# Kernel tuning notes

Hardware: AMD Instinct MI355X
Metric: run time of the kernel (lower is better)

Reference implementation:

```python
import jax, jax.numpy as jnp
from jax import lax
import numpy as np

T = 8
TAU = 2.0       # LIFNode tau
VTH = 1.0       # v_threshold for IF and LIF
ALPHA = 2.0     # surrogate.ATan default alpha
BN_EPS = 1e-5

# --- ATan surrogate-gradient heaviside (spikingjelly semantics) ---
@jax.custom_vjp
def heaviside_atan(x):
    return (x >= 0.0).astype(x.dtype)

def _h_fwd(x):
    return heaviside_atan(x), x

def _h_bwd(x, g):
    sg = (ALPHA / 2.0) / (1.0 + (jnp.pi / 2.0 * ALPHA * x) ** 2)
    return (g * sg,)

heaviside_atan.defvjp(_h_fwd, _h_bwd)

# --- multi-step IF node: v += x; spike; hard reset to 0 ---
def if_node(x_seq):
    def step(v, x):
        v = v + x
        s = heaviside_atan(v - VTH)
        return (1.0 - s) * v, s
    return lax.scan(step, jnp.zeros_like(x_seq[0]), x_seq)[1]

# --- multi-step LIF node (decay_input=True, v_reset=0, hard reset) ---
def lif_node(x_seq):
    def step(v, x):
        v = v + (x - v) / TAU
        s = heaviside_atan(v - VTH)
        return (1.0 - s) * v, s
    return lax.scan(step, jnp.zeros_like(x_seq[0]), x_seq)[1]

def conv2d(x, w, b):
    y = lax.conv_general_dilated(x, w, (1, 1), 'SAME', dimension_numbers=('NCHW', 'OIHW', 'NCHW'))
    return y + b[None, :, None, None]

def bn(x, g, b, m, v):
    scale = g * lax.rsqrt(v + BN_EPS)
    return (x - m[None, :, None, None]) * scale[None, :, None, None] + b[None, :, None, None]

def maxpool2(x):
    return lax.reduce_window(x, -jnp.inf, lax.max, (1, 1, 2, 2), (1, 1, 2, 2), 'VALID')


def setup_inputs():
    key = jax.random.key(0)
    ks = jax.random.split(key, 8)
    B = 32
    f32 = jnp.float32
    d = {}
    d['x'] = jax.random.normal(ks[0], (B, 1, 48, 48), f32)
    d['conv1_w'] = jax.random.normal(ks[1], (128, 1, 3, 3), f32) * 0.2
    d['conv1_b'] = jnp.zeros((128,), f32)
    d['bn1_g'] = jnp.ones((128,), f32)
    d['bn1_b'] = jnp.zeros((128,), f32)
    d['bn1_m'] = jnp.zeros((128,), f32)
    d['bn1_v'] = jnp.ones((128,), f32)
    d['conv2_w'] = jax.random.normal(ks[2], (128, 128, 3, 3), f32) * 0.03
    d['conv2_b'] = jnp.zeros((128,), f32)
    d['bn2_g'] = jnp.ones((128,), f32)
    d['bn2_b'] = jnp.zeros((128,), f32)
    d['bn2_m'] = jnp.zeros((128,), f32)
    d['bn2_v'] = jnp.ones((128,), f32)
    d['fc1_w'] = jax.random.normal(ks[3], (1152, 128 * 12 * 12), f32) * 0.007
    d['fc1_b'] = jnp.zeros((1152,), f32)
    d['fc2_w'] = jax.random.normal(ks[4], (128, 1152), f32) * 0.03
    d['fc2_b'] = jnp.zeros((128,), f32)
    d['fc3_w'] = jax.random.normal(ks[5], (7, 128), f32) * 0.09
    d['fc3_b'] = jnp.zeros((7,), f32)
    return d


def reference(x, conv1_w, conv1_b, bn1_g, bn1_b, bn1_m, bn1_v,
              conv2_w, conv2_b, bn2_g, bn2_b, bn2_m, bn2_v,
              fc1_w, fc1_b, fc2_w, fc2_b, fc3_w, fc3_b):
    B = x.shape[0]
    # layer1 (single-step): conv + BN (eval-mode), dropout is identity at eval
    h = bn(conv2d(x, conv1_w, conv1_b), bn1_g, bn1_b, bn1_m, bn1_v)  # [B,128,48,48]
    # repeat over T timesteps
    x_step = jnp.broadcast_to(h, (T,) + h.shape)                      # [T,B,128,48,48]
    # layer2: IF -> maxpool -> conv -> BN -> IF -> maxpool
    s1 = if_node(x_step)                                              # [T,B,128,48,48]
    p1 = maxpool2(s1.reshape((T * B,) + s1.shape[2:]))                # [T*B,128,24,24]
    c2 = bn(conv2d(p1, conv2_w, conv2_b), bn2_g, bn2_b, bn2_m, bn2_v)
    s2 = if_node(c2.reshape((T, B) + c2.shape[1:]))                   # [T,B,128,24,24]
    p2 = maxpool2(s2.reshape((T * B,) + s2.shape[2:]))                # [T*B,128,12,12]
    # layer3: flatten -> fc -> LIF -> fc -> LIF -> fc -> LIF
    f = p2.reshape(T, B, -1)                                          # [T,B,18432]
    l1 = lif_node(jnp.einsum('tbi,oi->tbo', f, fc1_w) + fc1_b)        # [T,B,1152]
    l2 = lif_node(jnp.einsum('tbi,oi->tbo', l1, fc2_w) + fc2_b)       # [T,B,128]
    l3 = lif_node(jnp.einsum('tbi,oi->tbo', l2, fc3_w) + fc3_b)       # [T,B,7]
    return l3.mean(axis=0)                                            # [B,7]
```

## Files before the change

kernel.cpp:

```cpp
#include <hip/hip_runtime.h>


typedef float  f32x4  __attribute__((ext_vector_type(4)));
typedef __bf16 bf16x8 __attribute__((ext_vector_type(8)));
typedef short  short8 __attribute__((ext_vector_type(8)));

#define T_STEPS 8
#define BATCH 32

static const size_t OFF_P1    = 0;
static const size_t OFF_PART  = 0;
static const size_t OFF_Y2    = 44302336;
static const size_t OFF_L1PRE = 44302336;
static const size_t OFF_L1S   = 45481984;
static const size_t OFF_L2PRE = 46661632;
static const size_t OFF_L2S   = 46792704;
static const size_t OFF_WT    = 119799808;
static const size_t OFF_P2    = 120389632;
static const size_t OFF_W2T   = 129826816;

__device__ __forceinline__ unsigned short bf16_rne(float f) {
  unsigned u = __builtin_bit_cast(unsigned, f);
  u += 0x7FFFu + ((u >> 16) & 1u);
  return (unsigned short)(u >> 16);
}
__device__ __forceinline__ float bf16_to_f(unsigned short h) {
  unsigned u = ((unsigned)h) << 16;
  return __builtin_bit_cast(float, u);
}

__device__ __forceinline__ void lds_load16(const void* g, void* l) {
  auto* gp = reinterpret_cast<const __attribute__((address_space(1))) unsigned int*>(
      reinterpret_cast<uintptr_t>(g));
  auto* lp = reinterpret_cast<__attribute__((address_space(3))) unsigned int*>(
      reinterpret_cast<uintptr_t>(l));
  __builtin_amdgcn_global_load_lds(gp, lp, 16, 0, 0);
}

__global__ __launch_bounds__(256) void zerofill(uint4* p, int n4) {
  int i = blockIdx.x * 256 + threadIdx.x;
  if (i < n4) p[i] = make_uint4(0u, 0u, 0u, 0u);
}

__global__ __launch_bounds__(256) void prep_weights(const float* __restrict__ conv2_w,
                                                    const float* __restrict__ fc2_w,
                                                    short* __restrict__ wt_hi,
                                                    short* __restrict__ wt_lo,
                                                    float* __restrict__ w2t) {
  int i = blockIdx.x * 256 + threadIdx.x;
  if (i < 147456) {
    int tap = i >> 14;
    int oc  = (i >> 7) & 127;
    int ic  = i & 127;
    float wv = conv2_w[oc * 1152 + ic * 9 + tap];
    unsigned short h = bf16_rne(wv);
    float lf = wv - bf16_to_f(h);
    wt_hi[i] = (short)h;
    wt_lo[i] = (short)bf16_rne(lf);
  } else {
    int j = i - 147456;
    int o = j & 127, k = j >> 7;
    w2t[j] = fc2_w[o * 1152 + k];
  }
}

__global__ __launch_bounds__(128) void conv1_if_pool(
    const float* __restrict__ x, const float* __restrict__ w1, const float* __restrict__ b1,
    const float* __restrict__ g1, const float* __restrict__ be1, const float* __restrict__ m1,
    const float* __restrict__ vv1, short* __restrict__ p1) {
  __shared__ float patch[16];
  const int c  = threadIdx.x;
  const int sp = blockIdx.x;
  const int b  = blockIdx.y;
  const int oy = sp / 24, ox = sp % 24;
  if (c < 16) {
    int py = c >> 2, px = c & 3;
    int iy = 2 * oy - 1 + py, ix = 2 * ox - 1 + px;
    float v = 0.f;
    if (iy >= 0 && iy < 48 && ix >= 0 && ix < 48) v = x[b * 2304 + iy * 48 + ix];
    patch[c] = v;
  }
  __syncthreads();
  float w[9];
#pragma unroll
  for (int i = 0; i < 9; ++i) w[i] = w1[c * 9 + i];
  float scale = g1[c] * rsqrtf(vv1[c] + 1e-5f);
  float shift = (b1[c] - m1[c]) * scale + be1[c];
  float h[4];
#pragma unroll
  for (int p = 0; p < 4; ++p) {
    int py = p >> 1, px = p & 1;
    float s = 0.f;
#pragma unroll
    for (int dy = 0; dy < 3; ++dy)
#pragma unroll
      for (int dx = 0; dx < 3; ++dx) s += patch[(py + dy) * 4 + (px + dx)] * w[dy * 3 + dx];
    h[p] = s * scale + shift;
  }
  float va = 0.f, vb = 0.f, vc = 0.f, vd = 0.f;
  size_t base = ((size_t)b * 676 + (size_t)(1 + oy) * 26 + (1 + ox)) * 128 + c;
#pragma unroll
  for (int t = 0; t < T_STEPS; ++t) {
    va += h[0]; vb += h[1]; vc += h[2]; vd += h[3];
    bool s0 = va >= 1.f, s1 = vb >= 1.f, s2 = vc >= 1.f, s3 = vd >= 1.f;
    p1[base + (size_t)t * (32 * 676 * 128)] = (s0 | s1 | s2 | s3) ? (short)0x3F80 : (short)0;
    if (s0) va = 0.f; if (s1) vb = 0.f; if (s2) vc = 0.f; if (s3) vd = 0.f;
  }
}

__global__ __launch_bounds__(256) void conv2_gemm(
    const short* __restrict__ p1pad, const short* __restrict__ wt_hi, const short* __restrict__ wt_lo,
    const float* __restrict__ conv2_b, const float* __restrict__ bn2_g, const float* __restrict__ bn2_b,
    const float* __restrict__ bn2_m, const float* __restrict__ bn2_v, float* __restrict__ y2) {
  __shared__ __align__(16) short lds[24576];
  short* ldsA = lds;
  short* ldsBh = lds + 8192;
  short* ldsBl = lds + 16384;

  const int tid = threadIdx.x;
  const int lane = tid & 63;
  const int w = tid >> 6;
  const int wm = w & 1, wn = w >> 1;
  const int m0 = blockIdx.x * 128;

  const int g = (lane & 7) ^ (lane >> 3);
  int rowofs[4], bofs[4];
#pragma unroll
  for (int j = 0; j < 4; ++j) {
    int r = w * 32 + j * 8 + (lane >> 3);
    int m = m0 + r;
    int tb = m / 576;
    int rem = m - tb * 576;
    int yy = rem / 24;
    int xx = rem - yy * 24;
    rowofs[j] = (tb * 676 + yy * 26 + xx) * 128 + g * 8;
    bofs[j] = r * 128 + g * 8;
  }

  f32x4 acc[4][4];
#pragma unroll
  for (int mi = 0; mi < 4; ++mi)
#pragma unroll
    for (int ni = 0; ni < 4; ++ni) acc[mi][ni] = (f32x4){0.f, 0.f, 0.f, 0.f};

#pragma unroll 1
  for (int s = 0; s < 18; ++s) {
    const int tap = s >> 1;
    const int kk = (s & 1) << 6;
    const int tapoff = ((tap / 3) * 26 + (tap % 3)) * 128;
    __syncthreads();
#pragma unroll
    for (int j = 0; j < 4; ++j) {
      lds_load16(p1pad + rowofs[j] + tapoff + kk, ldsA + (w * 32 + j * 8) * 64 + lane * 8);
    }
    const int wtoff = tap * 16384 + kk;
#pragma unroll
    for (int j = 0; j < 4; ++j) {
      lds_load16(wt_hi + wtoff + bofs[j], ldsBh + (w * 32 + j * 8) * 64 + lane * 8);
      lds_load16(wt_lo + wtoff + bofs[j], ldsBl + (w * 32 + j * 8) * 64 + lane * 8);
    }
    __syncthreads();
#pragma unroll
    for (int ks = 0; ks < 2; ++ks) {
      bf16x8 a[4], bh[4], bl[4];
      const int cch = ks * 4 + (lane >> 4);
#pragma unroll
      for (int i = 0; i < 4; ++i) {
        int r = wm * 64 + i * 16 + (lane & 15);
        a[i] = *(const bf16x8*)(ldsA + r * 64 + ((cch ^ (r & 7)) * 8));
        int n = wn * 64 + i * 16 + (lane & 15);
        bh[i] = *(const bf16x8*)(ldsBh + n * 64 + ((cch ^ (n & 7)) * 8));
        bl[i] = *(const bf16x8*)(ldsBl + n * 64 + ((cch ^ (n & 7)) * 8));
      }
#pragma unroll
      for (int mi = 0; mi < 4; ++mi)
#pragma unroll
        for (int ni = 0; ni < 4; ++ni) {
          acc[mi][ni] = __builtin_amdgcn_mfma_f32_16x16x32_bf16(a[mi], bh[ni], acc[mi][ni], 0, 0, 0);
          acc[mi][ni] = __builtin_amdgcn_mfma_f32_16x16x32_bf16(a[mi], bl[ni], acc[mi][ni], 0, 0, 0);
        }
    }
  }
#pragma unroll
  for (int ni = 0; ni < 4; ++ni) {
    int oc = wn * 64 + ni * 16 + (lane & 15);
    float sc = bn2_g[oc] * rsqrtf(bn2_v[oc] + 1e-5f);
    float sh = (conv2_b[oc] - bn2_m[oc]) * sc + bn2_b[oc];
#pragma unroll
    for (int mi = 0; mi < 4; ++mi) {
#pragma unroll
      for (int r = 0; r < 4; ++r) {
        int m = m0 + wm * 64 + mi * 16 + ((lane >> 4) << 2) + r;
        y2[(size_t)m * 128 + oc] = acc[mi][ni][r] * sc + sh;
      }
    }
  }
}

__global__ __launch_bounds__(128) void if2_pool(const float* __restrict__ y2, short* __restrict__ p2) {
  const int oc = threadIdx.x;
  const int gid = blockIdx.x;
  const int b = blockIdx.y;
  const int oy = gid / 3;
  const int ox0 = (gid % 3) * 4;
  float v[16];
#pragma unroll
  for (int i = 0; i < 16; ++i) v[i] = 0.f;
#pragma unroll
  for (int t = 0; t < T_STEPS; ++t) {
    const float* base = y2 + ((size_t)(t * 32 + b) * 576) * 128 + oc;
    bool sp[16];
#pragma unroll
    for (int row = 0; row < 2; ++row) {
      int iy = 2 * oy + row;
#pragma unroll
      for (int col = 0; col < 8; ++col) {
        int ix = 2 * ox0 + col;
        float xx = base[(size_t)(iy * 24 + ix) * 128];
        int idx = row * 8 + col;
        v[idx] += xx;
        bool s = v[idx] >= 1.f;
        sp[idx] = s;
        if (s) v[idx] = 0.f;
      }
    }
    ushort4 o4;
    o4.x = (sp[0] | sp[1] | sp[8]  | sp[9])  ? 0x3F80 : 0;
    o4.y = (sp[2] | sp[3] | sp[10] | sp[11]) ? 0x3F80 : 0;
    o4.z = (sp[4] | sp[5] | sp[12] | sp[13]) ? 0x3F80 : 0;
    o4.w = (sp[6] | sp[7] | sp[14] | sp[15]) ? 0x3F80 : 0;
    *(ushort4*)((unsigned short*)p2 + ((size_t)(t * 32 + b) * 128 + oc) * 144 + oy * 12 + ox0) = o4;
  }
}

__global__ __launch_bounds__(512) void fc1_gemm(const short* __restrict__ p2,
                                                const float* __restrict__ fc1_w,
                                                float* __restrict__ part) {
  __shared__ __align__(16) short lds[32768];
  short* ldsA = lds;
  short* ldsBh = lds + 16384;
  short* ldsBl = lds + 24576;

  const int tid = threadIdx.x;
  const int lane = tid & 63;
  const int w = tid >> 6;
  const int wm = w & 3, wn = w >> 2;
  const int n0 = blockIdx.x * 128;
  const int kb = blockIdx.y * 576;

  const int g = (lane & 7) ^ (lane >> 3);
  int aofs[4];
#pragma unroll
  for (int j = 0; j < 4; ++j) {
    int r = w * 32 + j * 8 + (lane >> 3);
    aofs[j] = r * 18432 + g * 8;
  }
  const int bn = tid >> 2;
  const int c0 = (tid & 3) * 2;
  const float* wrow = fc1_w + (size_t)(n0 + bn) * 18432 + c0 * 8;
  const int bpos0 = (c0 ^ (bn & 7)) * 8;
  const int bpos1 = ((c0 + 1) ^ (bn & 7)) * 8;

  f32x4 acc[4][4];
#pragma unroll
  for (int mi = 0; mi < 4; ++mi)
#pragma unroll
    for (int ni = 0; ni < 4; ++ni) acc[mi][ni] = (f32x4){0.f, 0.f, 0.f, 0.f};

#pragma unroll 1
  for (int s = 0; s < 9; ++s) {
    const int koff = kb + s * 64;
    __syncthreads();
#pragma unroll
    for (int j = 0; j < 4; ++j) {
      lds_load16(p2 + aofs[j] + koff, ldsA + (w * 32 + j * 8) * 64 + lane * 8);
    }
    {
      const float4* wp = (const float4*)(wrow + koff);
      float4 q0 = wp[0], q1 = wp[1], q2 = wp[2], q3 = wp[3];
      float fv[16] = {q0.x, q0.y, q0.z, q0.w, q1.x, q1.y, q1.z, q1.w,
                      q2.x, q2.y, q2.z, q2.w, q3.x, q3.y, q3.z, q3.w};
      short8 h0, h1, l0, l1;
#pragma unroll
      for (int q = 0; q < 8; ++q) {
        unsigned short hh = bf16_rne(fv[q]);
        h0[q] = (short)hh;
        l0[q] = (short)bf16_rne(fv[q] - bf16_to_f(hh));
      }
#pragma unroll
      for (int q = 0; q < 8; ++q) {
        unsigned short hh = bf16_rne(fv[8 + q]);
        h1[q] = (short)hh;
        l1[q] = (short)bf16_rne(fv[8 + q] - bf16_to_f(hh));
      }
      *(short8*)(ldsBh + bn * 64 + bpos0) = h0;
      *(short8*)(ldsBh + bn * 64 + bpos1) = h1;
      *(short8*)(ldsBl + bn * 64 + bpos0) = l0;
      *(short8*)(ldsBl + bn * 64 + bpos1) = l1;
    }
    __syncthreads();
#pragma unroll
    for (int ks = 0; ks < 2; ++ks) {
      bf16x8 a[4], bh[4], bl[4];
      const int cch = ks * 4 + (lane >> 4);
#pragma unroll
      for (int i = 0; i < 4; ++i) {
        int r = wm * 64 + i * 16 + (lane & 15);
        a[i] = *(const bf16x8*)(ldsA + r * 64 + ((cch ^ (r & 7)) * 8));
        int n = wn * 64 + i * 16 + (lane & 15);
        bh[i] = *(const bf16x8*)(ldsBh + n * 64 + ((cch ^ (n & 7)) * 8));
        bl[i] = *(const bf16x8*)(ldsBl + n * 64 + ((cch ^ (n & 7)) * 8));
      }
#pragma unroll
      for (int mi = 0; mi < 4; ++mi)
#pragma unroll
        for (int ni = 0; ni < 4; ++ni) {
          acc[mi][ni] = __builtin_amdgcn_mfma_f32_16x16x32_bf16(a[mi], bh[ni], acc[mi][ni], 0, 0, 0);
          acc[mi][ni] = __builtin_amdgcn_mfma_f32_16x16x32_bf16(a[mi], bl[ni], acc[mi][ni], 0, 0, 0);
        }
    }
  }
  const size_t pbase = (size_t)(blockIdx.y * 9 + blockIdx.x) * 32768;
#pragma unroll
  for (int ni = 0; ni < 4; ++ni) {
    int j = wn * 64 + ni * 16 + (lane & 15);
#pragma unroll
    for (int mi = 0; mi < 4; ++mi) {
#pragma unroll
      for (int r = 0; r < 4; ++r) {
        int m = wm * 64 + mi * 16 + ((lane >> 4) << 2) + r;
        part[pbase + (size_t)m * 128 + j] = acc[mi][ni][r];
      }
    }
  }
}

__global__ __launch_bounds__(256) void fc1_reduce(const float* __restrict__ part,
                                                  const float* __restrict__ fc1_b,
                                                  float* __restrict__ l1pre) {
  int i = blockIdx.x * 256 + threadIdx.x;
  int m = i / 1152, n = i - m * 1152;
  int nt = n >> 7, j = n & 127;
  float s = fc1_b[n];
#pragma unroll 4
  for (int ks = 0; ks < 32; ++ks) s += part[(((size_t)ks * 9 + nt) * 256 + m) * 128 + j];
  l1pre[i] = s;
}

__global__ __launch_bounds__(256) void lif_kernel(const float* __restrict__ pre,
                                                  float* __restrict__ spk, int nper) {
  int i = blockIdx.x * 256 + threadIdx.x;
  if (i >= nper) return;
  float v = 0.f;
#pragma unroll
  for (int t = 0; t < T_STEPS; ++t) {
    float xx = pre[(size_t)t * nper + i];
    v += (xx - v) * 0.5f;
    bool s = v >= 1.f;
    spk[(size_t)t * nper + i] = s ? 1.f : 0.f;
    if (s) v = 0.f;
  }
}

__global__ __launch_bounds__(128) void fc2_kernel(const float* __restrict__ l1s,
                                                  const float* __restrict__ w2t,
                                                  const float* __restrict__ b2,
                                                  float* __restrict__ l2pre) {
  __shared__ float sx[4608];
  const int tid = threadIdx.x;
  const int m0 = blockIdx.x * 4;
  for (int i = tid; i < 4608; i += 128) sx[i] = l1s[(size_t)m0 * 1152 + i];
  __syncthreads();
  float a0 = 0.f, a1 = 0.f, a2 = 0.f, a3 = 0.f;
  for (int k = 0; k < 1152; ++k) {
    float wv = w2t[k * 128 + tid];
    a0 += sx[k] * wv;
    a1 += sx[1152 + k] * wv;
    a2 += sx[2304 + k] * wv;
    a3 += sx[3456 + k] * wv;
  }
  float bb = b2[tid];
  l2pre[(size_t)(m0 + 0) * 128 + tid] = a0 + bb;
  l2pre[(size_t)(m0 + 1) * 128 + tid] = a1 + bb;
  l2pre[(size_t)(m0 + 2) * 128 + tid] = a2 + bb;
  l2pre[(size_t)(m0 + 3) * 128 + tid] = a3 + bb;
}

__global__ __launch_bounds__(64) void fc3_tail(const float* __restrict__ l2s,
                                               const float* __restrict__ w3,
                                               const float* __restrict__ b3,
                                               float* __restrict__ out) {
  const int o = blockIdx.x, b = blockIdx.y;
  const int lane = threadIdx.x;
  float wa = w3[o * 128 + lane], wb = w3[o * 128 + 64 + lane];
  float bias = b3[o];
  float v = 0.f, accum = 0.f;
#pragma unroll
  for (int t = 0; t < T_STEPS; ++t) {
    const float* row = l2s + ((size_t)t * 32 + b) * 128;
    float p = row[lane] * wa + row[64 + lane] * wb;
#pragma unroll
    for (int msk = 32; msk > 0; msk >>= 1) p += __shfl_xor(p, msk);
    float xx = p + bias;
    v += (xx - v) * 0.5f;
    bool s = v >= 1.f;
    accum += s ? 1.f : 0.f;
    if (s) v = 0.f;
  }
  if (lane == 0) out[b * 7 + o] = accum * 0.125f;
}

extern "C" void kernel_launch(void* const* d_in, const int* in_sizes, int n_in,
                              void* d_out, int out_size, void* d_ws, size_t ws_size,
                              hipStream_t stream) {
  const float* x       = (const float*)d_in[0];
  const float* conv1_w = (const float*)d_in[1];
  const float* conv1_b = (const float*)d_in[2];
  const float* bn1_g   = (const float*)d_in[3];
  const float* bn1_b   = (const float*)d_in[4];
  const float* bn1_m   = (const float*)d_in[5];
  const float* bn1_v   = (const float*)d_in[6];
  const float* conv2_w = (const float*)d_in[7];
  const float* conv2_b = (const float*)d_in[8];
  const float* bn2_g   = (const float*)d_in[9];
  const float* bn2_b   = (const float*)d_in[10];
  const float* bn2_m   = (const float*)d_in[11];
  const float* bn2_v   = (const float*)d_in[12];
  const float* fc1_w   = (const float*)d_in[13];
  const float* fc1_b   = (const float*)d_in[14];
  const float* fc2_w   = (const float*)d_in[15];
  const float* fc2_b   = (const float*)d_in[16];
  const float* fc3_w   = (const float*)d_in[17];
  const float* fc3_b   = (const float*)d_in[18];

  char* ws = (char*)d_ws;
  short* p1pad = (short*)(ws + OFF_P1);
  float* y2    = (float*)(ws + OFF_Y2);
  short* wt_hi = (short*)(ws + OFF_WT);
  short* wt_lo = wt_hi + 147456;
  short* p2    = (short*)(ws + OFF_P2);
  float* part  = (float*)(ws + OFF_PART);
  float* l1pre = (float*)(ws + OFF_L1PRE);
  float* l1s   = (float*)(ws + OFF_L1S);
  float* l2pre = (float*)(ws + OFF_L2PRE);
  float* l2s   = (float*)(ws + OFF_L2S);
  float* w2t   = (float*)(ws + OFF_W2T);
  float* out   = (float*)d_out;

  zerofill<<<10816, 256, 0, stream>>>((uint4*)p1pad, 2768896);
  prep_weights<<<1152, 256, 0, stream>>>(conv2_w, fc2_w, wt_hi, wt_lo, w2t);
  conv1_if_pool<<<dim3(576, 32), 128, 0, stream>>>(x, conv1_w, conv1_b, bn1_g, bn1_b, bn1_m, bn1_v, p1pad);
  conv2_gemm<<<1152, 256, 0, stream>>>(p1pad, wt_hi, wt_lo, conv2_b, bn2_g, bn2_b, bn2_m, bn2_v, y2);
  if2_pool<<<dim3(36, 32), 128, 0, stream>>>(y2, p2);
  fc1_gemm<<<dim3(9, 32), 512, 0, stream>>>(p2, fc1_w, part);
  fc1_reduce<<<1152, 256, 0, stream>>>(part, fc1_b, l1pre);
  lif_kernel<<<144, 256, 0, stream>>>(l1pre, l1s, 36864);
  fc2_kernel<<<64, 128, 0, stream>>>(l1s, w2t, fc2_b, l2pre);
  lif_kernel<<<16, 256, 0, stream>>>(l2pre, l2s, 4096);
  fc3_tail<<<dim3(7, 32), 64, 0, stream>>>(l2s, fc3_w, fc3_b, out);
}
```

Measured before the change: 404.5 us.

## Fuse IF2+maxpool into conv2 epilogue and merge small LIF/zero-fill kernels

Remaps conv2 GEMM tiles so each block covers all 8 timesteps of a 2x8 spatial patch for one batch. The IF neuron and 2x2 maxpool then run in the epilogue through LDS, so the large fp32 y2 intermediate is never written or re-read. The full p1pad zero-fill becomes a border-only zero-fill inside the weight prep kernel. The fc1 reduction is fused with LIF1, and LIF2 is folded into fc3_tail. This removes several launches and global round trips, at the cost of a serialized epilogue where only half the threads run the IF loop.

```diff
diff --git a/kernel.cpp b/kernel.cpp
--- a/kernel.cpp
+++ b/kernel.cpp
@@ -6,18 +6,14 @@
 typedef short  short8 __attribute__((ext_vector_type(8)));
 
 #define T_STEPS 8
-#define BATCH 32
 
 static const size_t OFF_P1    = 0;
 static const size_t OFF_PART  = 0;
-static const size_t OFF_Y2    = 44302336;
-static const size_t OFF_L1PRE = 44302336;
-static const size_t OFF_L1S   = 45481984;
-static const size_t OFF_L2PRE = 46661632;
-static const size_t OFF_L2S   = 46792704;
-static const size_t OFF_WT    = 119799808;
-static const size_t OFF_P2    = 120389632;
-static const size_t OFF_W2T   = 129826816;
+static const size_t OFF_WT    = 44302336;
+static const size_t OFF_P2    = 44892160;
+static const size_t OFF_W2T   = 54329344;
+static const size_t OFF_L1S   = 54919168;
+static const size_t OFF_L2PRE = 56098816;
 
 __device__ __forceinline__ unsigned short bf16_rne(float f) {
   unsigned u = __builtin_bit_cast(unsigned, f);
@@ -37,16 +33,12 @@
   __builtin_amdgcn_global_load_lds(gp, lp, 16, 0, 0);
 }
 
-__global__ __launch_bounds__(256) void zerofill(uint4* p, int n4) {
-  int i = blockIdx.x * 256 + threadIdx.x;
-  if (i < n4) p[i] = make_uint4(0u, 0u, 0u, 0u);
-}
-
-__global__ __launch_bounds__(256) void prep_weights(const float* __restrict__ conv2_w,
-                                                    const float* __restrict__ fc2_w,
-                                                    short* __restrict__ wt_hi,
-                                                    short* __restrict__ wt_lo,
-                                                    float* __restrict__ w2t) {
+__global__ __launch_bounds__(256) void prep(const float* __restrict__ conv2_w,
+                                            const float* __restrict__ fc2_w,
+                                            short* __restrict__ wt_hi,
+                                            short* __restrict__ wt_lo,
+                                            float* __restrict__ w2t,
+                                            uint4* __restrict__ p1pad4) {
   int i = blockIdx.x * 256 + threadIdx.x;
   if (i < 147456) {
     int tap = i >> 14;
@@ -54,13 +46,22 @@
     int ic  = i & 127;
     float wv = conv2_w[oc * 1152 + ic * 9 + tap];
     unsigned short h = bf16_rne(wv);
-    float lf = wv - bf16_to_f(h);
     wt_hi[i] = (short)h;
-    wt_lo[i] = (short)bf16_rne(lf);
-  } else {
+    wt_lo[i] = (short)bf16_rne(wv - bf16_to_f(h));
+  } else if (i < 294912) {
     int j = i - 147456;
     int o = j & 127, k = j >> 7;
     w2t[j] = fc2_w[o * 1152 + k];
+  } else if (i < 704512) {
+    int k = i - 294912;
+    int tb = k / 1600;
+    int rem = k - tb * 1600;
+    int pos = rem >> 4, c8 = rem & 15;
+    int y, x;
+    if (pos < 26)      { y = 0;  x = pos; }
+    else if (pos < 52) { y = 25; x = pos - 26; }
+    else { int jj = pos - 52; y = 1 + (jj >> 1); x = (jj & 1) * 25; }
+    p1pad4[(tb * 676 + y * 26 + x) * 16 + c8] = make_uint4(0u, 0u, 0u, 0u);
   }
 }
 
@@ -111,7 +112,7 @@
 __global__ __launch_bounds__(256) void conv2_gemm(
     const short* __restrict__ p1pad, const short* __restrict__ wt_hi, const short* __restrict__ wt_lo,
     const float* __restrict__ conv2_b, const float* __restrict__ bn2_g, const float* __restrict__ bn2_b,
-    const float* __restrict__ bn2_m, const float* __restrict__ bn2_v, float* __restrict__ y2) {
+    const float* __restrict__ bn2_m, const float* __restrict__ bn2_v, short* __restrict__ p2) {
   __shared__ __align__(16) short lds[24576];
   short* ldsA = lds;
   short* ldsBh = lds + 8192;
@@ -121,19 +122,17 @@
   const int lane = tid & 63;
   const int w = tid >> 6;
   const int wm = w & 1, wn = w >> 1;
-  const int m0 = blockIdx.x * 128;
+  const int b = blockIdx.y;
+  const int py = blockIdx.x / 3;
+  const int pxq = blockIdx.x - py * 3;
 
   const int g = (lane & 7) ^ (lane >> 3);
   int rowofs[4], bofs[4];
 #pragma unroll
   for (int j = 0; j < 4; ++j) {
     int r = w * 32 + j * 8 + (lane >> 3);
-    int m = m0 + r;
-    int tb = m / 576;
-    int rem = m - tb * 576;
-    int yy = rem / 24;
-    int xx = rem - yy * 24;
-    rowofs[j] = (tb * 676 + yy * 26 + xx) * 128 + g * 8;
+    int t = r >> 4, iy = (r >> 3) & 1, ix = r & 7;
+    rowofs[j] = (((t * 32 + b) * 676) + (2 * py + iy) * 26 + (pxq * 8 + ix)) * 128 + g * 8;
     bofs[j] = r * 128 + g * 8;
   }
 
@@ -181,55 +180,63 @@
         }
     }
   }
+
+  float sc[4], sh[4];
 #pragma unroll
   for (int ni = 0; ni < 4; ++ni) {
     int oc = wn * 64 + ni * 16 + (lane & 15);
-    float sc = bn2_g[oc] * rsqrtf(bn2_v[oc] + 1e-5f);
-    float sh = (conv2_b[oc] - bn2_m[oc]) * sc + bn2_b[oc];
-#pragma unroll
-    for (int mi = 0; mi < 4; ++mi) {
-#pragma unroll
-      for (int r = 0; r < 4; ++r) {
-        int m = m0 + wm * 64 + mi * 16 + ((lane >> 4) << 2) + r;
-        y2[(size_t)m * 128 + oc] = acc[mi][ni][r] * sc + sh;
-      }
-    }
-  }
-}
-
-__global__ __launch_bounds__(128) void if2_pool(const float* __restrict__ y2, short* __restrict__ p2) {
-  const int oc = threadIdx.x;
-  const int gid = blockIdx.x;
-  const int b = blockIdx.y;
-  const int oy = gid / 3;
-  const int ox0 = (gid % 3) * 4;
-  float v[16];
-#pragma unroll
-  for (int i = 0; i < 16; ++i) v[i] = 0.f;
-#pragma unroll
-  for (int t = 0; t < T_STEPS; ++t) {
-    const float* base = y2 + ((size_t)(t * 32 + b) * 576) * 128 + oc;
-    bool sp[16];
-#pragma unroll
-    for (int row = 0; row < 2; ++row) {
-      int iy = 2 * oy + row;
-#pragma unroll
-      for (int col = 0; col < 8; ++col) {
-        int ix = 2 * ox0 + col;
-        float xx = base[(size_t)(iy * 24 + ix) * 128];
-        int idx = row * 8 + col;
-        v[idx] += xx;
-        bool s = v[idx] >= 1.f;
-        sp[idx] = s;
-        if (s) v[idx] = 0.f;
-      }
-    }
-    ushort4 o4;
-    o4.x = (sp[0] | sp[1] | sp[8]  | sp[9])  ? 0x3F80 : 0;
-    o4.y = (sp[2] | sp[3] | sp[10] | sp[11]) ? 0x3F80 : 0;
-    o4.z = (sp[4] | sp[5] | sp[12] | sp[13]) ? 0x3F80 : 0;
-    o4.w = (sp[6] | sp[7] | sp[14] | sp[15]) ? 0x3F80 : 0;
-    *(ushort4*)((unsigned short*)p2 + ((size_t)(t * 32 + b) * 128 + oc) * 144 + oy * 12 + ox0) = o4;
+    sc[ni] = bn2_g[oc] * rsqrtf(bn2_v[oc] + 1e-5f);
+    sh[ni] = (conv2_b[oc] - bn2_m[oc]) * sc[ni] + bn2_b[oc];
+  }
+  float* ybuf = (float*)lds;
+  const int S = 132;
+  float vst[16];
+#pragma unroll
+  for (int q = 0; q < 16; ++q) vst[q] = 0.f;
+  unsigned short* p2u = (unsigned short*)p2;
+  __syncthreads();
+#pragma unroll 1
+  for (int half = 0; half < 2; ++half) {
+    if (wm == half) {
+#pragma unroll
+      for (int ni = 0; ni < 4; ++ni)
+#pragma unroll
+        for (int mi = 0; mi < 4; ++mi)
+#pragma unroll
+          for (int r = 0; r < 4; ++r) {
+            int row = mi * 16 + ((lane >> 4) << 2) + r;
+            int col = wn * 64 + ni * 16 + (lane & 15);
+            ybuf[row * S + col] = acc[mi][ni][r] * sc[ni] + sh[ni];
+          }
+    }
+    __syncthreads();
+    if (tid < 128) {
+      const int oc = tid;
+#pragma unroll
+      for (int tau = 0; tau < 4; ++tau) {
+        int t = half * 4 + tau;
+        unsigned short ov[4];
+#pragma unroll
+        for (int gx = 0; gx < 4; ++gx) {
+          bool any = false;
+#pragma unroll
+          for (int iy = 0; iy < 2; ++iy)
+#pragma unroll
+            for (int j = 0; j < 2; ++j) {
+              float xx = ybuf[(tau * 16 + iy * 8 + 2 * gx + j) * S + oc];
+              int q = gx * 4 + iy * 2 + j;
+              vst[q] += xx;
+              bool s = vst[q] >= 1.f;
+              any |= s;
+              if (s) vst[q] = 0.f;
+            }
+          ov[gx] = any ? (unsigned short)0x3F80 : (unsigned short)0;
+        }
+        ushort4 o4; o4.x = ov[0]; o4.y = ov[1]; o4.z = ov[2]; o4.w = ov[3];
+        *(ushort4*)(p2u + ((size_t)(t * 32 + b) * 128 + oc) * 144 + py * 12 + pxq * 4) = o4;
+      }
+    }
+    __syncthreads();
   }
 }
 
@@ -335,30 +342,24 @@
   }
 }
 
-__global__ __launch_bounds__(256) void fc1_reduce(const float* __restrict__ part,
-                                                  const float* __restrict__ fc1_b,
-                                                  float* __restrict__ l1pre) {
-  int i = blockIdx.x * 256 + threadIdx.x;
-  int m = i / 1152, n = i - m * 1152;
+__global__ __launch_bounds__(128) void fc1_reduce_lif(const float* __restrict__ part,
+                                                      const float* __restrict__ fc1_b,
+                                                      float* __restrict__ l1s) {
+  int i = blockIdx.x * 128 + threadIdx.x;
+  int b = i / 1152, n = i - b * 1152;
   int nt = n >> 7, j = n & 127;
-  float s = fc1_b[n];
-#pragma unroll 4
-  for (int ks = 0; ks < 32; ++ks) s += part[(((size_t)ks * 9 + nt) * 256 + m) * 128 + j];
-  l1pre[i] = s;
-}
-
-__global__ __launch_bounds__(256) void lif_kernel(const float* __restrict__ pre,
-                                                  float* __restrict__ spk, int nper) {
-  int i = blockIdx.x * 256 + threadIdx.x;
-  if (i >= nper) return;
+  float bias = fc1_b[n];
   float v = 0.f;
 #pragma unroll
   for (int t = 0; t < T_STEPS; ++t) {
-    float xx = pre[(size_t)t * nper + i];
-    v += (xx - v) * 0.5f;
-    bool s = v >= 1.f;
-    spk[(size_t)t * nper + i] = s ? 1.f : 0.f;
-    if (s) v = 0.f;
+    int m = t * 32 + b;
+    float s = bias;
+#pragma unroll 8
+    for (int ks = 0; ks < 32; ++ks) s += part[(((size_t)ks * 9 + nt) * 256 + m) * 128 + j];
+    v += (s - v) * 0.5f;
+    bool sp = v >= 1.f;
+    l1s[(size_t)m * 1152 + n] = sp ? 1.f : 0.f;
+    if (sp) v = 0.f;
   }
 }
 
@@ -386,7 +387,7 @@
   l2pre[(size_t)(m0 + 3) * 128 + tid] = a3 + bb;
 }
 
-__global__ __launch_bounds__(64) void fc3_tail(const float* __restrict__ l2s,
+__global__ __launch_bounds__(64) void fc3_tail(const float* __restrict__ l2pre,
                                                const float* __restrict__ w3,
                                                const float* __restrict__ b3,
                                                float* __restrict__ out) {
@@ -394,11 +395,16 @@
   const int lane = threadIdx.x;
   float wa = w3[o * 128 + lane], wb = w3[o * 128 + 64 + lane];
   float bias = b3[o];
-  float v = 0.f, accum = 0.f;
+  float va = 0.f, vb = 0.f, v = 0.f, accum = 0.f;
 #pragma unroll
   for (int t = 0; t < T_STEPS; ++t) {
-    const float* row = l2s + ((size_t)t * 32 + b) * 128;
-    float p = row[lane] * wa + row[64 + lane] * wb;
+    const float* row = l2pre + ((size_t)(t * 32 + b)) * 128;
+    float xa = row[lane], xb = row[64 + lane];
+    va += (xa - va) * 0.5f;
+    bool sa = va >= 1.f; if (sa) va = 0.f;
+    vb += (xb - vb) * 0.5f;
+    bool sb = vb >= 1.f; if (sb) vb = 0.f;
+    float p = (sa ? wa : 0.f) + (sb ? wb : 0.f);
 #pragma unroll
     for (int msk = 32; msk > 0; msk >>= 1) p += __shfl_xor(p, msk);
     float xx = p + bias;
@@ -435,27 +441,20 @@
 
   char* ws = (char*)d_ws;
   short* p1pad = (short*)(ws + OFF_P1);
-  float* y2    = (float*)(ws + OFF_Y2);
+  float* part  = (float*)(ws + OFF_PART);
   short* wt_hi = (short*)(ws + OFF_WT);
   short* wt_lo = wt_hi + 147456;
   short* p2    = (short*)(ws + OFF_P2);
-  float* part  = (float*)(ws + OFF_PART);
-  float* l1pre = (float*)(ws + OFF_L1PRE);
+  float* w2t   = (float*)(ws + OFF_W2T);
   float* l1s   = (float*)(ws + OFF_L1S);
   float* l2pre = (float*)(ws + OFF_L2PRE);
-  float* l2s   = (float*)(ws + OFF_L2S);
-  float* w2t   = (float*)(ws + OFF_W2T);
   float* out   = (float*)d_out;
 
-  zerofill<<<10816, 256, 0, stream>>>((uint4*)p1pad, 2768896);
-  prep_weights<<<1152, 256, 0, stream>>>(conv2_w, fc2_w, wt_hi, wt_lo, w2t);
+  prep<<<2752, 256, 0, stream>>>(conv2_w, fc2_w, wt_hi, wt_lo, w2t, (uint4*)p1pad);
   conv1_if_pool<<<dim3(576, 32), 128, 0, stream>>>(x, conv1_w, conv1_b, bn1_g, bn1_b, bn1_m, bn1_v, p1pad);
-  conv2_gemm<<<1152, 256, 0, stream>>>(p1pad, wt_hi, wt_lo, conv2_b, bn2_g, bn2_b, bn2_m, bn2_v, y2);
-  if2_pool<<<dim3(36, 32), 128, 0, stream>>>(y2, p2);
+  conv2_gemm<<<dim3(36, 32), 256, 0, stream>>>(p1pad, wt_hi, wt_lo, conv2_b, bn2_g, bn2_b, bn2_m, bn2_v, p2);
   fc1_gemm<<<dim3(9, 32), 512, 0, stream>>>(p2, fc1_w, part);
-  fc1_reduce<<<1152, 256, 0, stream>>>(part, fc1_b, l1pre);
-  lif_kernel<<<144, 256, 0, stream>>>(l1pre, l1s, 36864);
+  fc1_reduce_lif<<<288, 128, 0, stream>>>(part, fc1_b, l1s);
   fc2_kernel<<<64, 128, 0, stream>>>(l1s, w2t, fc2_b, l2pre);
-  lif_kernel<<<16, 256, 0, stream>>>(l2pre, l2s, 4096);
-  fc3_tail<<<dim3(7, 32), 64, 0, stream>>>(l2s, fc3_w, fc3_b, out);
-}
+  fc3_tail<<<dim3(7, 32), 64, 0, stream>>>(l2pre, fc3_w, fc3_b, out);
+}
```

Result: faster. 392.9 us (-2.9%).
